# Kernel tuning notes

Measured on AMD Instinct MI355X. Metric: run time of the kernel, lower is better.

Reference implementation:

```python
import jax, jax.numpy as jnp
import numpy as np
from jax import lax

EPS = 1e-07
B, NPRIM, NSEC, DP, DS = 512, 1152, 10, 8, 16


def setup_inputs() -> dict:
    key = jax.random.key(0)
    ks = jax.random.split(key, 12)
    inp = {}
    inp['x'] = jax.random.uniform(ks[0], (B, 28, 28, 1), dtype=jnp.float32)
    inp['labels'] = jax.random.randint(ks[1], (B,), 0, NSEC)
    # conv1: 9x9, 1 -> 256, relu ; conv2 (primary caps): 9x9 stride2, 256 -> 256
    inp['conv1_k'] = jax.random.normal(ks[2], (9, 9, 1, 256), dtype=jnp.float32) * 0.05
    inp['conv1_b'] = jnp.zeros((256,), dtype=jnp.float32)
    inp['conv2_k'] = jax.random.normal(ks[3], (9, 9, 256, 256), dtype=jnp.float32) * 0.02
    inp['conv2_b'] = jnp.zeros((256,), dtype=jnp.float32)
    # pose transform W: [1152, 10, 16, 8]
    inp['w'] = jax.random.normal(ks[4], (NPRIM, NSEC, DS, DP), dtype=jnp.float32) * 0.05
    # decoder
    inp['d1_w'] = jax.random.normal(ks[5], (NSEC * DS, 512), dtype=jnp.float32) * 0.05
    inp['d1_b'] = jnp.zeros((512,), dtype=jnp.float32)
    inp['d2_w'] = jax.random.normal(ks[6], (512, 1024), dtype=jnp.float32) * 0.05
    inp['d2_b'] = jnp.zeros((1024,), dtype=jnp.float32)
    inp['d3_w'] = jax.random.normal(ks[7], (1024, 784), dtype=jnp.float32) * 0.05
    inp['d3_b'] = jnp.zeros((784,), dtype=jnp.float32)
    return inp


def _conv(x, k, b, stride):
    y = lax.conv_general_dilated(x, k, (stride, stride), 'VALID',
                                 dimension_numbers=('NHWC', 'HWIO', 'NHWC'))
    return y + b


def _squash(s):
    # s: [..., D]
    s_norm = jnp.linalg.norm(s, axis=-1, keepdims=True)
    sq = jnp.square(s_norm)
    return sq / (1.0 + sq) * s / (s_norm + EPS)


def reference(x, labels, conv1_k, conv1_b, conv2_k, conv2_b, w,
              d1_w, d1_b, d2_w, d2_b, d3_w, d3_b):
    h = jax.nn.relu(_conv(x, conv1_k, conv1_b, 1))        # [B,20,20,256]
    p = _conv(h, conv2_k, conv2_b, 2)                      # [B,6,6,256]
    u = p.reshape(x.shape[0], NPRIM, DP)                   # [B,1152,8]
    # u_hat[b,n,s,d] = sum_p w[n,s,d,p] * u[b,n,p]
    u_hat = jnp.einsum('nsdp,bnp->bnsd', w, u)             # [B,1152,10,16]

    b_logits = jnp.zeros((x.shape[0], NPRIM, NSEC, 1), dtype=u_hat.dtype)
    v = None
    for _ in range(3):  # r routing iterations (fixed, small)
        c = jax.nn.softmax(b_logits, axis=-2)              # softmax over 10 secondary caps
        s = jnp.sum(c * u_hat, axis=1, keepdims=True)      # [B,1,10,16]
        v = _squash(s)                                     # [B,1,10,16]
        agreement = jnp.sum(u_hat * v, axis=-1, keepdims=True)  # [B,1152,10,1]
        b_logits = b_logits + agreement

    y = jax.nn.one_hot(labels, NSEC, dtype=v.dtype)        # [B,10]
    mask = y[:, None, :, None]                             # [B,1,10,1]
    v_masked = mask * v
    v_flat = v_masked.reshape(-1, NSEC * DS)               # [B,160]
    r1 = jax.nn.relu(v_flat @ d1_w + d1_b)
    r2 = jax.nn.relu(r1 @ d2_w + d2_b)
    recon = jax.nn.sigmoid(r2 @ d3_w + d3_b)               # [B,784]
    return v, recon
```

## Files before the change

kernel.cpp:

```cpp
#include <hip/hip_runtime.h>

#define USH unsigned short

__device__ inline float bf2f(USH u){ return __uint_as_float(((unsigned)u)<<16); }
__device__ inline USH f2bf(float f){
  unsigned u = __float_as_uint(f);
  return (USH)((u + 0x7FFFu + ((u>>16)&1u))>>16);
}

typedef __attribute__((ext_vector_type(8))) short bf16x8;
typedef __attribute__((ext_vector_type(4))) float f32x4;

__device__ inline void gll16(const USH* g, USH* l){
  __builtin_amdgcn_global_load_lds((const __attribute__((address_space(1))) void*)g,
                                   (__attribute__((address_space(3))) void*)l, 16, 0, 0);
}

__global__ __launch_bounds__(256) void im2col_k(
    const float* __restrict__ x, USH* __restrict__ xcol)
{
  int b = blockIdx.x, t = threadIdx.x;
  __shared__ float xs[784];
  for (int i = t; i < 784; i += 256) xs[i] = x[b*784 + i];
  __syncthreads();
  USH* dst = xcol + (size_t)b*38400;
  for (int idx = t; idx < 38400; idx += 256) {
    int sp = idx / 96, k = idx - sp*96;
    int y = sp / 20, xx = sp - y*20;
    USH v = 0;
    if (k < 81) {
      int dy = k / 9, dx = k - dy*9;
      v = f2bf(xs[(y+dy)*28 + xx + dx]);
    }
    dst[idx] = v;
  }
}

__global__ __launch_bounds__(256) void tr_k1(const float* __restrict__ k1, USH* __restrict__ k1T)
{
  int n = threadIdx.x;
  for (int k = 0; k < 96; ++k)
    k1T[n*96 + k] = (k < 81) ? f2bf(k1[k*256 + n]) : (USH)0;
}

__global__ __launch_bounds__(256) void gemm1(
    const USH* __restrict__ xcol, const USH* __restrict__ k1T,
    const float* __restrict__ b1, USH* __restrict__ h)
{
  int t = threadIdx.x;
  int m0 = blockIdx.x * 64;
  int lane = t & 63, wave = t >> 6;
  int wn = wave * 64;
  int fr = lane & 15, fq = lane >> 4;

  f32x4 acc[4][4];
#pragma unroll
  for (int i = 0; i < 4; ++i)
#pragma unroll
    for (int j = 0; j < 4; ++j)
#pragma unroll
      for (int r = 0; r < 4; ++r) acc[i][j][r] = 0.f;

#pragma unroll
  for (int kt = 0; kt < 3; ++kt) {
    int kc = kt*32 + fq*8;
    bf16x8 af[4], bg[4];
#pragma unroll
    for (int mf = 0; mf < 4; ++mf)
      af[mf] = *(const bf16x8*)&xcol[(size_t)(m0 + mf*16 + fr)*96 + kc];
#pragma unroll
    for (int nf = 0; nf < 4; ++nf)
      bg[nf] = *(const bf16x8*)&k1T[(size_t)(wn + nf*16 + fr)*96 + kc];
#pragma unroll
    for (int mf = 0; mf < 4; ++mf)
#pragma unroll
      for (int nf = 0; nf < 4; ++nf)
        acc[mf][nf] = __builtin_amdgcn_mfma_f32_16x16x32_bf16(af[mf], bg[nf], acc[mf][nf], 0,0,0);
  }

#pragma unroll
  for (int mf = 0; mf < 4; ++mf)
#pragma unroll
    for (int nf = 0; nf < 4; ++nf) {
      int n = wn + nf*16 + fr;
      float bias = b1[n];
#pragma unroll
      for (int r = 0; r < 4; ++r) {
        int m = m0 + mf*16 + fq*4 + r;
        float v = acc[mf][nf][r] + bias;
        h[(size_t)m*256 + n] = f2bf(v > 0.f ? v : 0.f);
      }
    }
}

__global__ __launch_bounds__(256) void tr_k2(const float* __restrict__ k2, USH* __restrict__ k2T)
{
  __shared__ float tile[32][33];
  int kb = blockIdx.x*32, nb = blockIdx.y*32;
  int tx = threadIdx.x & 31, ty = threadIdx.x >> 5;
#pragma unroll
  for (int r = 0; r < 4; ++r) {
    int k = kb + ty + r*8;
    tile[ty + r*8][tx] = k2[(size_t)k*256 + nb + tx];
  }
  __syncthreads();
#pragma unroll
  for (int r = 0; r < 4; ++r) {
    int n = nb + ty + r*8;
    k2T[(size_t)n*20736 + kb + tx] = f2bf(tile[tx][ty + r*8]);
  }
}

__global__ __launch_bounds__(256) void conv2_mfma(
    const USH* __restrict__ h, const USH* __restrict__ k2T,
    float* __restrict__ up)
{
  __shared__ __align__(16) USH Asm[2][128*64];
  __shared__ __align__(16) USH Bsm[2][64*64];
  int t = threadIdx.x;
  int flat = blockIdx.x;
  int xcd  = flat & 7;
  int slot = flat >> 3;
  int nb   = slot & 3;
  int rest = slot >> 2;
  int mb_l = rest % 18;
  int ksl  = rest / 18;
  int mb   = xcd*18 + mb_l;

  int sg = (((t&7) ^ ((t>>3)&7)) << 3);

  int arow_off[4];
#pragma unroll
  for (int i = 0; i < 4; ++i) {
    int row = (t>>3) + i*32;
    int m = mb*128 + row;
    int bb = m/36, r = m - bb*36;
    int oy = r/6, ox = r - oy*6;
    arow_off[i] = bb*102400 + oy*10240 + ox*512 + sg;
  }
  int brow_off[2];
#pragma unroll
  for (int i = 0; i < 2; ++i) {
    int nl = (t>>3) + i*32;
    brow_off[i] = (nb*64 + nl)*20736 + sg;
  }

  int lane = t & 63;
  int wave = t >> 6;
  int wm = (wave>>1)*64, wn = (wave&1)*32;
  int fr = lane & 15, fq = lane >> 4;

  f32x4 acc[4][2];
#pragma unroll
  for (int i = 0; i < 4; ++i)
#pragma unroll
    for (int j = 0; j < 2; ++j)
#pragma unroll
      for (int r = 0; r < 4; ++r) acc[i][j][r] = 0.f;

  int rg0 = (((0*4 + fq) ^ (fr&7)) << 3);
  int rg1 = (((1*4 + fq) ^ (fr&7)) << 3);

#define STAGE(buf, kt) do {                                            \
    int j_ = (kt) >> 2;                                                \
    int cin0_ = ((kt) & 3) << 6;                                       \
    int dy_ = j_/9, dx_ = j_ - dy_*9;                                  \
    int koff_ = (dy_*20 + dx_)*256 + cin0_;                            \
    USH* Ad_ = &Asm[buf][(t>>6)*512];                                  \
    USH* Bd_ = &Bsm[buf][(t>>6)*512];                                  \
    _Pragma("unroll")                                                  \
    for (int i_ = 0; i_ < 4; ++i_) gll16(h + arow_off[i_] + koff_, Ad_ + i_*2048); \
    _Pragma("unroll")                                                  \
    for (int i_ = 0; i_ < 2; ++i_) gll16(k2T + brow_off[i_] + (kt)*64, Bd_ + i_*2048); \
  } while(0)

  const int k0 = ksl*81, kend = k0 + 81;
  STAGE(0, k0);
  __syncthreads();

  int cur = 0;
  for (int kt = k0; kt < kend; ++kt) {
    if (kt + 1 < kend) STAGE(cur^1, kt+1);

    bf16x8 af[4][2], bg[2][2];
#pragma unroll
    for (int mf = 0; mf < 4; ++mf) {
      af[mf][0] = *(const bf16x8*)&Asm[cur][(wm + mf*16 + fr)*64 + rg0];
      af[mf][1] = *(const bf16x8*)&Asm[cur][(wm + mf*16 + fr)*64 + rg1];
    }
#pragma unroll
    for (int nf = 0; nf < 2; ++nf) {
      bg[nf][0] = *(const bf16x8*)&Bsm[cur][(wn + nf*16 + fr)*64 + rg0];
      bg[nf][1] = *(const bf16x8*)&Bsm[cur][(wn + nf*16 + fr)*64 + rg1];
    }
#pragma unroll
    for (int mf = 0; mf < 4; ++mf)
#pragma unroll
      for (int nf = 0; nf < 2; ++nf) {
        acc[mf][nf] = __builtin_amdgcn_mfma_f32_16x16x32_bf16(af[mf][0], bg[nf][0], acc[mf][nf], 0,0,0);
        acc[mf][nf] = __builtin_amdgcn_mfma_f32_16x16x32_bf16(af[mf][1], bg[nf][1], acc[mf][nf], 0,0,0);
      }
    __syncthreads();
    cur ^= 1;
  }
#undef STAGE

  float* dst = up + (size_t)ksl*4718592;
#pragma unroll
  for (int mf = 0; mf < 4; ++mf)
#pragma unroll
    for (int nf = 0; nf < 2; ++nf) {
      int n = nb*64 + wn + nf*16 + fr;
#pragma unroll
      for (int r = 0; r < 4; ++r) {
        int m = mb*128 + wm + mf*16 + fq*4 + r;
        dst[(size_t)m*256 + n] = acc[mf][nf][r];
      }
    }
}

__global__ __launch_bounds__(256) void reduce_u(
    const float* __restrict__ up, const float* __restrict__ b2, float* __restrict__ u)
{
  int i = blockIdx.x*256 + threadIdx.x;
  f32x4 a = *(const f32x4*)&up[(size_t)i*4];
  f32x4 b = *(const f32x4*)&up[4718592ull + (size_t)i*4];
  f32x4 c = *(const f32x4*)&up[9437184ull + (size_t)i*4];
  f32x4 d = *(const f32x4*)&up[14155776ull + (size_t)i*4];
  int n0 = (i*4) & 255;
  f32x4 o;
#pragma unroll
  for (int j = 0; j < 4; ++j) o[j] = (a[j] + b[j]) + (c[j] + d[j]) + b2[n0 + j];
  *(f32x4*)&u[(size_t)i*4] = o;
}

__global__ __launch_bounds__(192) void wsum_tr(const float* __restrict__ w,
    float* __restrict__ Ws)
{
  int n = blockIdx.x, t = threadIdx.x;
  __shared__ float wn[1280];
  for (int i = t; i < 1280; i += 192) wn[i] = w[n*1280 + i];
  __syncthreads();
  if (t < 160) {
#pragma unroll
    for (int p = 0; p < 8; ++p)
      Ws[((size_t)n*8 + p)*160 + t] = wn[(t>>4)*128 + (t&15)*8 + p];
  }
}

__global__ __launch_bounds__(192) void p1gemm(const float* __restrict__ u,
    const float* __restrict__ Ws, float* __restrict__ part)
{
  int b0 = blockIdx.x*32, k0 = blockIdx.y*288;
  int t = threadIdx.x;
  __shared__ float usm[288*36];
  for (int i = t; i < 288*32; i += 192) {
    int bl = i/288, kk = i - bl*288;
    usm[kk*36 + bl] = u[(size_t)(b0+bl)*9216 + k0 + kk];
  }
  __syncthreads();
  if (t < 160) {
    const float* wp = Ws + (size_t)k0*160 + t;
#pragma unroll 1
    for (int half = 0; half < 2; ++half) {
      float acc[16];
#pragma unroll
      for (int i = 0; i < 16; ++i) acc[i] = 0.f;
      for (int kk = 0; kk < 288; ++kk) {
        float wv = wp[(size_t)kk*160];
        const f32x4* ub = (const f32x4*)&usm[kk*36 + half*16];
        f32x4 u0 = ub[0], u1 = ub[1], u2 = ub[2], u3 = ub[3];
#pragma unroll
        for (int i = 0; i < 4; ++i) {
          acc[i]    += u0[i]*wv;
          acc[4+i]  += u1[i]*wv;
          acc[8+i]  += u2[i]*wv;
          acc[12+i] += u3[i]*wv;
        }
      }
      float* pp = &part[((size_t)blockIdx.y*512 + b0 + half*16)*160 + t];
#pragma unroll
      for (int i = 0; i < 16; ++i) pp[(size_t)i*160] = acc[i];
    }
  }
}

__global__ __launch_bounds__(192) void squash1(const float* __restrict__ part,
    float* __restrict__ vout)
{
  int b = blockIdx.x, t = threadIdx.x;
  if (t < 160) {
    float sv = 0.f;
    for (int ks = 0; ks < 32; ++ks) sv += part[((size_t)ks*512 + b)*160 + t];
    sv *= 0.1f;
    float n2 = sv*sv;
    n2 += __shfl_xor(n2, 1, 16);
    n2 += __shfl_xor(n2, 2, 16);
    n2 += __shfl_xor(n2, 4, 16);
    n2 += __shfl_xor(n2, 8, 16);
    float nrm = sqrtf(n2);
    float o = (n2/(1.f + n2)) * sv / (nrm + 1e-7f);
    vout[b*160 + t] = o;
  }
}

__global__ __launch_bounds__(256) void uhat_kernel(
    const float* __restrict__ u, const float* __restrict__ w, USH* __restrict__ uh)
{
  int n = blockIdx.x, b0 = blockIdx.y*64;
  int t = threadIdx.x;
  __shared__ float wsm[20*65];
  __shared__ float usm[512];
  for (int i = t; i < 1280; i += 256) wsm[(i>>6)*65 + (i&63)] = w[n*1280 + i];
  for (int i = t; i < 512; i += 256) {
    int bl = i>>3, p = i&7;
    usm[i] = u[(size_t)(b0+bl)*9216 + n*8 + p];
  }
  __syncthreads();
  USH* dst = uh + ((size_t)n*512 + b0)*160;
  for (int v = t; v < 1280; v += 256) {
    int bl = v/20, oct = v - bl*20;
    const float* upt = &usm[bl*8];
    bf16x8 pk;
#pragma unroll
    for (int j = 0; j < 8; ++j) {
      const float* wp = &wsm[oct*65 + j*8];
      float a = 0.f;
#pragma unroll
      for (int p = 0; p < 8; ++p) a += wp[p]*upt[p];
      pk[j] = (short)f2bf(a);
    }
    *(bf16x8*)&dst[(size_t)v*8] = pk;
  }
}

__global__ __launch_bounds__(256) void route_part(
    const USH* __restrict__ uh, const float* __restrict__ vin,
    float* __restrict__ partR)
{
  int bc = blockIdx.x, nc = blockIdx.y;
  int b0 = bc*16, n0 = nc*48;
  int t = threadIdx.x;
  int bL = t >> 4, s = t & 15;
  bool act = s < 10;
  int b = b0 + bL;

  float vr[16];
#pragma unroll
  for (int d = 0; d < 16; ++d) vr[d] = 0.f;
  if (act) {
    const float* vp = vin + (size_t)b*160 + s*16;
#pragma unroll
    for (int d = 0; d < 16; ++d) vr[d] = vp[d];
  }
  float acc[16];
#pragma unroll
  for (int d = 0; d < 16; ++d) acc[d] = 0.f;

  const size_t nstride = (size_t)512*160;
  const USH* base = uh + ((size_t)n0*512 + b)*160 + s*16;

  bf16x8 c0{}, c1{};
  if (act) { c0 = *(const bf16x8*)base; c1 = *(const bf16x8*)(base + 8); }

  for (int ni = 0; ni < 48; ++ni) {
    bf16x8 f0 = c0, f1 = c1;
    if (ni + 1 < 48 && act) {
      const USH* p = base + (size_t)(ni+1)*nstride;
      f0 = *(const bf16x8*)p;
      f1 = *(const bf16x8*)(p + 8);
    }
    float uv[16];
    if (act) {
#pragma unroll
      for (int d = 0; d < 8; ++d) { uv[d] = bf2f((USH)c0[d]); uv[8+d] = bf2f((USH)c1[d]); }
    } else {
#pragma unroll
      for (int d = 0; d < 16; ++d) uv[d] = 0.f;
    }
    c0 = f0; c1 = f1;

    float dot = 0.f;
#pragma unroll
    for (int d = 0; d < 16; ++d) dot += uv[d]*vr[d];
    float lg = act ? dot : -1e30f;
    float mx = lg;
    mx = fmaxf(mx, __shfl_xor(mx, 1, 16));
    mx = fmaxf(mx, __shfl_xor(mx, 2, 16));
    mx = fmaxf(mx, __shfl_xor(mx, 4, 16));
    mx = fmaxf(mx, __shfl_xor(mx, 8, 16));
    float e = __expf(lg - mx);
    float sum = e;
    sum += __shfl_xor(sum, 1, 16);
    sum += __shfl_xor(sum, 2, 16);
    sum += __shfl_xor(sum, 4, 16);
    sum += __shfl_xor(sum, 8, 16);
    float c = e / sum;
#pragma unroll
    for (int d = 0; d < 16; ++d) acc[d] += c*uv[d];
  }

  if (act) {
    float* pp = &partR[((size_t)nc*512 + b)*160 + s*16];
#pragma unroll
    for (int q = 0; q < 4; ++q) {
      f32x4 o;
#pragma unroll
      for (int j = 0; j < 4; ++j) o[j] = acc[q*4 + j];
      *(f32x4*)(pp + q*4) = o;
    }
  }
}

template<int PASS>
__global__ __launch_bounds__(192) void squash_part(const float* __restrict__ partR,
    const float* __restrict__ vprev, float* __restrict__ vout, float* __restrict__ vext)
{
  int b = blockIdx.x, t = threadIdx.x;
  if (t < 160) {
    float sv = 0.f;
    for (int nc = 0; nc < 24; ++nc) sv += partR[((size_t)nc*512 + b)*160 + t];
    float n2 = sv*sv;
    n2 += __shfl_xor(n2, 1, 16);
    n2 += __shfl_xor(n2, 2, 16);
    n2 += __shfl_xor(n2, 4, 16);
    n2 += __shfl_xor(n2, 8, 16);
    float nrm = sqrtf(n2);
    float o = (n2/(1.f + n2)) * sv / (nrm + 1e-7f);
    vout[b*160 + t] = o;
    if (PASS == 2) vext[b*160 + t] = vprev[b*160 + t] + o;
    if (PASS == 3) vext[b*160 + t] = o;
  }
}

__global__ __launch_bounds__(512) void d1_kernel(const float* __restrict__ v3,
    const int* __restrict__ labels, const float* __restrict__ w,
    const float* __restrict__ bias, float* __restrict__ r1)
{
  int b = blockIdx.x; int j = threadIdx.x;
  int lb = labels[b];
  float acc = bias[j];
#pragma unroll
  for (int d = 0; d < 16; ++d)
    acc += v3[b*160 + lb*16 + d] * w[(lb*16 + d)*512 + j];
  r1[(size_t)b*512 + j] = acc > 0.f ? acc : 0.f;
}

__global__ __launch_bounds__(256) void d2_kernel(const float* __restrict__ a,
    const float* __restrict__ w, const float* __restrict__ bias, float* __restrict__ o)
{
  int j = blockIdx.x*256 + threadIdx.x;
  int b0 = blockIdx.y*4;
  __shared__ float as[4*512];
  for (int i = threadIdx.x; i < 4*512; i += 256) as[i] = a[(size_t)(b0 + (i>>9))*512 + (i&511)];
  __syncthreads();
  float acc[4];
  float bs = bias[j];
#pragma unroll
  for (int i = 0; i < 4; ++i) acc[i] = bs;
  for (int k = 0; k < 512; ++k) {
    float wv = w[(size_t)k*1024 + j];
#pragma unroll
    for (int i = 0; i < 4; ++i) acc[i] += as[i*512 + k]*wv;
  }
#pragma unroll
  for (int i = 0; i < 4; ++i)
    o[(size_t)(b0+i)*1024 + j] = acc[i] > 0.f ? acc[i] : 0.f;
}

__global__ __launch_bounds__(256) void d3_kernel(const float* __restrict__ a,
    const float* __restrict__ w, const float* __restrict__ bias, float* __restrict__ o)
{
  int j = blockIdx.x*256 + threadIdx.x;
  int b0 = blockIdx.y*4;
  __shared__ float as[4*1024];
  for (int i = threadIdx.x; i < 4*1024; i += 256) as[i] = a[(size_t)(b0 + (i>>10))*1024 + (i&1023)];
  __syncthreads();
  if (j < 784) {
    float acc[4];
    float bs = bias[j];
#pragma unroll
    for (int i = 0; i < 4; ++i) acc[i] = bs;
    for (int k = 0; k < 1024; ++k) {
      float wv = w[(size_t)k*784 + j];
#pragma unroll
      for (int i = 0; i < 4; ++i) acc[i] += as[i*1024 + k]*wv;
    }
#pragma unroll
    for (int i = 0; i < 4; ++i)
      o[(size_t)(b0+i)*784 + j] = 1.f/(1.f + __expf(-acc[i]));
  }
}

extern "C" void kernel_launch(void* const* d_in, const int* in_sizes, int n_in,
                              void* d_out, int out_size, void* d_ws, size_t ws_size,
                              hipStream_t stream)
{
  const float* x   = (const float*)d_in[0];
  const int*   lab = (const int*)  d_in[1];
  const float* k1  = (const float*)d_in[2];
  const float* b1  = (const float*)d_in[3];
  const float* k2  = (const float*)d_in[4];
  const float* b2  = (const float*)d_in[5];
  const float* w   = (const float*)d_in[6];
  const float* d1w = (const float*)d_in[7];
  const float* d1b = (const float*)d_in[8];
  const float* d2w = (const float*)d_in[9];
  const float* d2b = (const float*)d_in[10];
  const float* d3w = (const float*)d_in[11];
  const float* d3b = (const float*)d_in[12];
  float* out = (float*)d_out;

  char* ws = (char*)d_ws;
  USH*   uh    = (USH*)(ws + 0);
  USH*   h     = (USH*)(ws + 0);
  float* up    = (float*)(ws + 104857600ull);
  USH*   xcol  = (USH*)(ws + 142606336ull);
  float* u     = (float*)(ws + 188743680ull);
  USH*   k2T   = (USH*)(ws + 207618048ull);
  float* Wsum  = (float*)(ws + 207618048ull);
  float* part  = (float*)(ws + 218234880ull);
  float* partR = (float*)(ws + 218234880ull);
  USH*   k1T   = (USH*)(ws + 241827840ull);
  float* v1    = (float*)(ws + 242155520ull);
  float* v2    = (float*)(ws + 242483200ull);
  float* v3    = (float*)(ws + 242810880ull);
  float* vsum  = (float*)(ws + 243138560ull);
  float* r1    = (float*)(ws + 243466240ull);
  float* r2    = (float*)(ws + 244514816ull);

  im2col_k<<<512, 256, 0, stream>>>(x, xcol);
  tr_k1<<<1, 256, 0, stream>>>(k1, k1T);
  gemm1<<<3200, 256, 0, stream>>>(xcol, k1T, b1, h);

  tr_k2<<<dim3(648,8), 256, 0, stream>>>(k2, k2T);
  conv2_mfma<<<2304, 256, 0, stream>>>(h, k2T, up);
  reduce_u<<<4608, 256, 0, stream>>>(up, b2, u);

  wsum_tr<<<1152, 192, 0, stream>>>(w, Wsum);
  p1gemm<<<dim3(16,32), 192, 0, stream>>>(u, Wsum, part);
  squash1<<<512, 192, 0, stream>>>(part, v1);

  uhat_kernel<<<dim3(1152,8), 256, 0, stream>>>(u, w, uh);

  route_part<<<dim3(32,24), 256, 0, stream>>>(uh, v1, partR);
  squash_part<2><<<512, 192, 0, stream>>>(partR, v1, v2, vsum);
  route_part<<<dim3(32,24), 256, 0, stream>>>(uh, vsum, partR);
  squash_part<3><<<512, 192, 0, stream>>>(partR, nullptr, v3, out);

  d1_kernel<<<512, 512, 0, stream>>>(v3, lab, d1w, d1b, r1);
  d2_kernel<<<dim3(4,128), 256, 0, stream>>>(r1, d2w, d2b, r2);
  d3_kernel<<<dim3(4,128), 256, 0, stream>>>(r2, d3w, d3b, out + 81920);
}
```

Before: 602.2 us.

## Run decoder layers as bf16 MFMA GEMMs and deepen routing prefetch

New measurement: 595.5 us. About the same (-1.1%).

```diff
diff --git a/kernel.cpp b/kernel.cpp
--- a/kernel.cpp
+++ b/kernel.cpp
@@ -108,6 +108,26 @@
   for (int r = 0; r < 4; ++r) {
     int n = nb + ty + r*8;
     k2T[(size_t)n*20736 + kb + tx] = f2bf(tile[tx][ty + r*8]);
+  }
+}
+
+__global__ __launch_bounds__(256) void tr_dec(const float* __restrict__ in,
+    USH* __restrict__ outT, int K, int N, int limN)
+{
+  __shared__ float tile[32][33];
+  int kb = blockIdx.x*32, nb = blockIdx.y*32;
+  int tx = threadIdx.x & 31, ty = threadIdx.x >> 5;
+#pragma unroll
+  for (int r = 0; r < 4; ++r) {
+    int k = kb + ty + r*8;
+    int n = nb + tx;
+    tile[ty + r*8][tx] = (n < limN) ? in[(size_t)k*limN + n] : 0.f;
+  }
+  __syncthreads();
+#pragma unroll
+  for (int r = 0; r < 4; ++r) {
+    int n = nb + ty + r*8;
+    outT[(size_t)n*K + kb + tx] = f2bf(tile[tx][ty + r*8]);
   }
 }
 
@@ -360,13 +380,16 @@
   const size_t nstride = (size_t)512*160;
   const USH* base = uh + ((size_t)n0*512 + b)*160 + s*16;
 
-  bf16x8 c0{}, c1{};
-  if (act) { c0 = *(const bf16x8*)base; c1 = *(const bf16x8*)(base + 8); }
+  bf16x8 c0{}, c1{}, p0{}, p1{};
+  if (act) {
+    c0 = *(const bf16x8*)base;              c1 = *(const bf16x8*)(base + 8);
+    p0 = *(const bf16x8*)(base + nstride);  p1 = *(const bf16x8*)(base + nstride + 8);
+  }
 
   for (int ni = 0; ni < 48; ++ni) {
-    bf16x8 f0 = c0, f1 = c1;
-    if (ni + 1 < 48 && act) {
-      const USH* p = base + (size_t)(ni+1)*nstride;
+    bf16x8 f0 = p0, f1 = p1;
+    if (ni + 2 < 48 && act) {
+      const USH* p = base + (size_t)(ni+2)*nstride;
       f0 = *(const bf16x8*)p;
       f1 = *(const bf16x8*)(p + 8);
     }
@@ -378,7 +401,8 @@
 #pragma unroll
       for (int d = 0; d < 16; ++d) uv[d] = 0.f;
     }
-    c0 = f0; c1 = f1;
+    c0 = p0; c1 = p1;
+    p0 = f0; p1 = f1;
 
     float dot = 0.f;
 #pragma unroll
@@ -435,7 +459,7 @@
 
 __global__ __launch_bounds__(512) void d1_kernel(const float* __restrict__ v3,
     const int* __restrict__ labels, const float* __restrict__ w,
-    const float* __restrict__ bias, float* __restrict__ r1)
+    const float* __restrict__ bias, USH* __restrict__ r1b)
 {
   int b = blockIdx.x; int j = threadIdx.x;
   int lb = labels[b];
@@ -443,53 +467,64 @@
 #pragma unroll
   for (int d = 0; d < 16; ++d)
     acc += v3[b*160 + lb*16 + d] * w[(lb*16 + d)*512 + j];
-  r1[(size_t)b*512 + j] = acc > 0.f ? acc : 0.f;
-}
-
-__global__ __launch_bounds__(256) void d2_kernel(const float* __restrict__ a,
-    const float* __restrict__ w, const float* __restrict__ bias, float* __restrict__ o)
-{
-  int j = blockIdx.x*256 + threadIdx.x;
-  int b0 = blockIdx.y*4;
-  __shared__ float as[4*512];
-  for (int i = threadIdx.x; i < 4*512; i += 256) as[i] = a[(size_t)(b0 + (i>>9))*512 + (i&511)];
-  __syncthreads();
-  float acc[4];
-  float bs = bias[j];
-#pragma unroll
-  for (int i = 0; i < 4; ++i) acc[i] = bs;
-  for (int k = 0; k < 512; ++k) {
-    float wv = w[(size_t)k*1024 + j];
-#pragma unroll
-    for (int i = 0; i < 4; ++i) acc[i] += as[i*512 + k]*wv;
-  }
+  r1b[(size_t)b*512 + j] = f2bf(acc > 0.f ? acc : 0.f);
+}
+
+template<int MODE>
+__global__ __launch_bounds__(256) void gemm_dec(
+    const USH* __restrict__ A, const USH* __restrict__ Bt,
+    const float* __restrict__ bias, void* __restrict__ Cv,
+    int K, int limN)
+{
+  int t = threadIdx.x;
+  int m0 = blockIdx.x * 64;
+  int n0 = blockIdx.y * 256;
+  int lane = t & 63, wave = t >> 6;
+  int wn = n0 + wave * 64;
+  int fr = lane & 15, fq = lane >> 4;
+
+  f32x4 acc[4][4];
 #pragma unroll
   for (int i = 0; i < 4; ++i)
-    o[(size_t)(b0+i)*1024 + j] = acc[i] > 0.f ? acc[i] : 0.f;
-}
-
-__global__ __launch_bounds__(256) void d3_kernel(const float* __restrict__ a,
-    const float* __restrict__ w, const float* __restrict__ bias, float* __restrict__ o)
-{
-  int j = blockIdx.x*256 + threadIdx.x;
-  int b0 = blockIdx.y*4;
-  __shared__ float as[4*1024];
-  for (int i = threadIdx.x; i < 4*1024; i += 256) as[i] = a[(size_t)(b0 + (i>>10))*1024 + (i&1023)];
-  __syncthreads();
-  if (j < 784) {
-    float acc[4];
-    float bs = bias[j];
-#pragma unroll
-    for (int i = 0; i < 4; ++i) acc[i] = bs;
-    for (int k = 0; k < 1024; ++k) {
-      float wv = w[(size_t)k*784 + j];
-#pragma unroll
-      for (int i = 0; i < 4; ++i) acc[i] += as[i*1024 + k]*wv;
-    }
-#pragma unroll
-    for (int i = 0; i < 4; ++i)
-      o[(size_t)(b0+i)*784 + j] = 1.f/(1.f + __expf(-acc[i]));
-  }
+#pragma unroll
+    for (int j = 0; j < 4; ++j)
+#pragma unroll
+      for (int r = 0; r < 4; ++r) acc[i][j][r] = 0.f;
+
+  for (int kt = 0; kt < K/32; ++kt) {
+    int kc = kt*32 + fq*8;
+    bf16x8 af[4], bg[4];
+#pragma unroll
+    for (int mf = 0; mf < 4; ++mf)
+      af[mf] = *(const bf16x8*)&A[(size_t)(m0 + mf*16 + fr)*K + kc];
+#pragma unroll
+    for (int nf = 0; nf < 4; ++nf)
+      bg[nf] = *(const bf16x8*)&Bt[(size_t)(wn + nf*16 + fr)*K + kc];
+#pragma unroll
+    for (int mf = 0; mf < 4; ++mf)
+#pragma unroll
+      for (int nf = 0; nf < 4; ++nf)
+        acc[mf][nf] = __builtin_amdgcn_mfma_f32_16x16x32_bf16(af[mf], bg[nf], acc[mf][nf], 0,0,0);
+  }
+
+#pragma unroll
+  for (int mf = 0; mf < 4; ++mf)
+#pragma unroll
+    for (int nf = 0; nf < 4; ++nf) {
+      int n = wn + nf*16 + fr;
+      float bs = (n < limN) ? bias[n] : 0.f;
+#pragma unroll
+      for (int r = 0; r < 4; ++r) {
+        int m = m0 + mf*16 + fq*4 + r;
+        float v = acc[mf][nf][r] + bs;
+        if (MODE == 0) {
+          ((USH*)Cv)[(size_t)m*limN + n] = f2bf(v > 0.f ? v : 0.f);
+        } else {
+          if (n < limN)
+            ((float*)Cv)[(size_t)m*limN + n] = 1.f/(1.f + __expf(-v));
+        }
+      }
+    }
 }
 
 extern "C" void kernel_launch(void* const* d_in, const int* in_sizes, int n_in,
@@ -521,13 +556,15 @@
   float* Wsum  = (float*)(ws + 207618048ull);
   float* part  = (float*)(ws + 218234880ull);
   float* partR = (float*)(ws + 218234880ull);
+  USH*   d2wT  = (USH*)(ws + 233963520ull);
+  USH*   d3wT  = (USH*)(ws + 235012096ull);
+  USH*   r1b   = (USH*)(ws + 237109248ull);
+  USH*   r2b   = (USH*)(ws + 237633536ull);
   USH*   k1T   = (USH*)(ws + 241827840ull);
   float* v1    = (float*)(ws + 242155520ull);
   float* v2    = (float*)(ws + 242483200ull);
   float* v3    = (float*)(ws + 242810880ull);
   float* vsum  = (float*)(ws + 243138560ull);
-  float* r1    = (float*)(ws + 243466240ull);
-  float* r2    = (float*)(ws + 244514816ull);
 
   im2col_k<<<512, 256, 0, stream>>>(x, xcol);
   tr_k1<<<1, 256, 0, stream>>>(k1, k1T);
@@ -542,13 +579,16 @@
   squash1<<<512, 192, 0, stream>>>(part, v1);
 
   uhat_kernel<<<dim3(1152,8), 256, 0, stream>>>(u, w, uh);
+
+  tr_dec<<<dim3(16,32), 256, 0, stream>>>(d2w, d2wT, 512, 1024, 1024);
+  tr_dec<<<dim3(32,32), 256, 0, stream>>>(d3w, d3wT, 1024, 1024, 784);
 
   route_part<<<dim3(32,24), 256, 0, stream>>>(uh, v1, partR);
   squash_part<2><<<512, 192, 0, stream>>>(partR, v1, v2, vsum);
   route_part<<<dim3(32,24), 256, 0, stream>>>(uh, vsum, partR);
   squash_part<3><<<512, 192, 0, stream>>>(partR, nullptr, v3, out);
 
-  d1_kernel<<<512, 512, 0, stream>>>(v3, lab, d1w, d1b, r1);
-  d2_kernel<<<dim3(4,128), 256, 0, stream>>>(r1, d2w, d2b, r2);
-  d3_kernel<<<dim3(4,128), 256, 0, stream>>>(r2, d3w, d3b, out + 81920);
-}
+  d1_kernel<<<512, 512, 0, stream>>>(v3, lab, d1w, d1b, r1b);
+  gemm_dec<0><<<dim3(8,4), 256, 0, stream>>>(r1b, d2wT, d2b, r2b, 512, 1024);
+  gemm_dec<1><<<dim3(8,4), 256, 0, stream>>>(r2b, d3wT, d3b, out + 81920, 1024, 784);
+}
```
